# Kernel tuning notes

Measured on AMD Instinct MI355X. Metric: run time of the kernel, lower is better.

Reference implementation:

```python
import jax, jax.numpy as jnp
import numpy as np

D_MODEL = 1024
D_FF = 4 * D_MODEL
NUM_EXPERTS = 8
TOP_K = 2
BATCH, SEQ = 2, 2048


def setup_inputs() -> dict:
    key = jax.random.key(0)
    ks = jax.random.split(key, 6)
    s_in = 1.0 / np.sqrt(D_MODEL)
    s_ff = 1.0 / np.sqrt(D_FF)
    x = jax.random.normal(ks[0], (BATCH, SEQ, D_MODEL), dtype=jnp.float32)
    Wg = jax.random.uniform(ks[1], (D_MODEL, NUM_EXPERTS), minval=-s_in, maxval=s_in, dtype=jnp.float32)
    W1 = jax.random.uniform(ks[2], (NUM_EXPERTS, D_MODEL, D_FF), minval=-s_in, maxval=s_in, dtype=jnp.float32)
    b1 = jax.random.uniform(ks[3], (NUM_EXPERTS, D_FF), minval=-s_in, maxval=s_in, dtype=jnp.float32)
    W2 = jax.random.uniform(ks[4], (NUM_EXPERTS, D_FF, D_MODEL), minval=-s_ff, maxval=s_ff, dtype=jnp.float32)
    b2 = jax.random.uniform(ks[5], (NUM_EXPERTS, D_MODEL), minval=-s_ff, maxval=s_ff, dtype=jnp.float32)
    return {"x": x, "Wg": Wg, "W1": W1, "b1": b1, "W2": W2, "b2": b2}


def reference(x, Wg, W1, b1, W2, b2):
    B, S, D = x.shape
    x_flat = x.reshape(-1, D)                      # [T, D]
    gate_logits = x_flat @ Wg                      # [T, E] (eval mode: no noise)
    gate_probs = jax.nn.softmax(gate_logits, axis=-1)
    top_v, top_i = jax.lax.top_k(gate_probs, TOP_K)            # [T, k]
    top_v = top_v / (jnp.sum(top_v, axis=-1, keepdims=True) + 1e-8)
    out = jnp.zeros_like(x_flat)
    for e in range(NUM_EXPERTS):
        # combine weight for expert e: sum of normalized top-k probs routed here
        w_e = jnp.sum(jnp.where(top_i == e, top_v, 0.0), axis=-1)   # [T]
        h = jax.nn.gelu(x_flat @ W1[e] + b1[e], approximate=False)  # [T, F]
        y = h @ W2[e] + b2[e]                                       # [T, D]
        out = out + w_e[:, None] * y
    return out.reshape(B, S, D)
```

## Files before the change

kernel.cpp:

```cpp
#include <hip/hip_runtime.h>
#include <math.h>

typedef __attribute__((ext_vector_type(8))) short short8;
typedef __attribute__((ext_vector_type(4))) float f32x4;
typedef unsigned short u16;

#define NT 4096
#define DM 1024
#define DF 4096
#define NE 8
#define HROWS 9216
#define TIT 72
#define YROWS (2 * NT + 8)

static __device__ __forceinline__ u16 f2bf(float f) {
  union { float f; unsigned u; } v; v.f = f;
  return (u16)((v.u + 0x7fffu + ((v.u >> 16) & 1u)) >> 16);
}

static __device__ __forceinline__ void gload16(const void* g, void* l) {
  __builtin_amdgcn_global_load_lds((const __attribute__((address_space(1))) void*)g,
                                   (__attribute__((address_space(3))) void*)l, 16, 0, 0);
}

__global__ __launch_bounds__(256) void gate_k(const float* __restrict__ x,
                                              const float* __restrict__ Wg,
                                              int* __restrict__ te,
                                              float* __restrict__ tw) {
  int t = blockIdx.x * 4 + (threadIdx.x >> 6);
  int l = threadIdx.x & 63;
  float a0=0,a1=0,a2=0,a3=0,a4=0,a5=0,a6=0,a7=0;
  const float* xr = x + (size_t)t * DM;
  for (int k = l; k < DM; k += 64) {
    float xv = xr[k];
    const float4* wp = (const float4*)(Wg + k * 8);
    float4 w0 = wp[0], w1 = wp[1];
    a0 += xv * w0.x; a1 += xv * w0.y; a2 += xv * w0.z; a3 += xv * w0.w;
    a4 += xv * w1.x; a5 += xv * w1.y; a6 += xv * w1.z; a7 += xv * w1.w;
  }
#pragma unroll
  for (int s = 32; s >= 1; s >>= 1) {
    a0 += __shfl_down(a0, s); a1 += __shfl_down(a1, s);
    a2 += __shfl_down(a2, s); a3 += __shfl_down(a3, s);
    a4 += __shfl_down(a4, s); a5 += __shfl_down(a5, s);
    a6 += __shfl_down(a6, s); a7 += __shfl_down(a7, s);
  }
  if (l == 0) {
    float lg[8] = {a0,a1,a2,a3,a4,a5,a6,a7};
    float m = lg[0];
#pragma unroll
    for (int e = 1; e < 8; ++e) m = fmaxf(m, lg[e]);
    float p[8], s = 0.f;
#pragma unroll
    for (int e = 0; e < 8; ++e) { p[e] = expf(lg[e] - m); s += p[e]; }
#pragma unroll
    for (int e = 0; e < 8; ++e) p[e] /= s;
    int i0 = 0; float v0 = p[0];
#pragma unroll
    for (int e = 1; e < 8; ++e) if (p[e] > v0) { v0 = p[e]; i0 = e; }
    int i1 = -1; float v1 = -1.f;
#pragma unroll
    for (int e = 0; e < 8; ++e) {
      if (e == i0) continue;
      if (p[e] > v1) { v1 = p[e]; i1 = e; }
    }
    float norm = v0 + v1 + 1e-8f;
    te[t*2]   = i0; te[t*2+1] = i1;
    tw[t*2]   = v0 / norm; tw[t*2+1] = v1 / norm;
  }
}

__global__ __launch_bounds__(256) void route_k(const int* __restrict__ te,
                                               const float* __restrict__ tw,
                                               int* __restrict__ meta,
                                               int* __restrict__ lt,
                                               float* __restrict__ lw) {
  int i = blockIdx.x * 256 + threadIdx.x;
  if (i >= NT * 2) return;
  int e = te[i];
  float w = tw[i];
  int pos = atomicAdd(&meta[e], 1);
  lt[e * NT + pos] = i;
  lw[e * NT + pos] = w;
}

__global__ __launch_bounds__(256) void finalize_k(int* __restrict__ meta,
                                                  int* __restrict__ lt,
                                                  float* __restrict__ lw) {
  __shared__ int s_cnt[8], s_pc[8];
  if (threadIdx.x == 0) {
    int base = 0, nt_ = 0;
    for (int e = 0; e < 8; ++e) {
      int c = meta[e];
      int pc = (c + 127) & ~127;
      s_cnt[e] = c; s_pc[e] = pc;
      meta[8 + e] = pc;
      meta[16 + e] = base;
      base += pc;
      for (int mt = 0; mt < pc / 128; ++mt) meta[32 + nt_++] = (e << 16) | mt;
    }
    meta[24] = nt_;
  }
  __syncthreads();
  for (int e = 0; e < 8; ++e) {
    int c = s_cnt[e], pc = s_pc[e];
    for (int i = c + (int)threadIdx.x; i < pc; i += 256) {
      lt[e * NT + i] = 2 * NT;
      lw[e * NT + i] = 0.f;
    }
  }
}

__global__ __launch_bounds__(256) void prep_x(const float* __restrict__ x, u16* __restrict__ xbf) {
  size_t i = (size_t)blockIdx.x * 256 + threadIdx.x;
  const float4* p = (const float4*)(x + i * 8);
  float4 a = p[0], b = p[1];
  short8 o = { (short)f2bf(a.x), (short)f2bf(a.y), (short)f2bf(a.z), (short)f2bf(a.w),
               (short)f2bf(b.x), (short)f2bf(b.y), (short)f2bf(b.z), (short)f2bf(b.w) };
  *(short8*)(xbf + i * 8) = o;
}

__global__ __launch_bounds__(256) void prep_wT(const float* __restrict__ in,
                                               u16* __restrict__ out, int K, int N) {
  const int e = blockIdx.z;
  const int n0 = blockIdx.x * 64, k0 = blockIdx.y * 64;
  const float* ie = in + (size_t)e * K * N;
  u16* oe = out + (size_t)e * K * N;
  __shared__ u16 t[64 * 72];
  const int tid = threadIdx.x;
  const int kr = tid >> 4, nq = (tid & 15) * 4;
#pragma unroll
  for (int it = 0; it < 4; ++it) {
    int k = it * 16 + kr;
    float4 v = *(const float4*)(ie + (size_t)(k0 + k) * N + n0 + nq);
    t[(nq + 0) * 72 + k] = f2bf(v.x);
    t[(nq + 1) * 72 + k] = f2bf(v.y);
    t[(nq + 2) * 72 + k] = f2bf(v.z);
    t[(nq + 3) * 72 + k] = f2bf(v.w);
  }
  __syncthreads();
#pragma unroll
  for (int it = 0; it < 2; ++it) {
    int idx = it * 256 + tid;
    int n = idx >> 3, kc = idx & 7;
    short8 v = *(const short8*)&t[n * 72 + kc * 8];
    *(short8*)(oe + (size_t)(n0 + n) * K + k0 + kc * 8) = v;
  }
}

#define STAGE4(b)                                            \
  do {                                                       \
    gload16(pa0, laA + (b) * 4096 + lda0);                   \
    gload16(pa1, laA + (b) * 4096 + lda1);                   \
    gload16(pb0, laB + (b) * 4096 + lda0);                   \
    gload16(pb1, laB + (b) * 4096 + lda1);                   \
    pa0 += 32; pa1 += 32; pb0 += 32; pb1 += 32;              \
  } while (0)

__global__ __launch_bounds__(256) void ffn1_k(const u16* __restrict__ xbf,
                                              const u16* __restrict__ W1T,
                                              const float* __restrict__ b1,
                                              const int* __restrict__ lt,
                                              const int* __restrict__ meta,
                                              u16* __restrict__ H) {
  const int nt = blockIdx.x;
  const int ti = blockIdx.y;
  if (ti >= meta[24]) return;
  const int em = meta[32 + ti];
  const int e = em >> 16, mt = em & 0xffff;
  const int rbase = meta[16 + e];

  __shared__ u16 As[2 * 4096];
  __shared__ u16 Bs[2 * 4096];

  const int tid = threadIdx.x, lane = tid & 63, wv = tid >> 6;
  const int wm = wv >> 1, wn = wv & 1, l15 = lane & 15, l4 = lane >> 4;

  int r0i = tid >> 2, s0 = tid & 3;
  int r1i = (256 + tid) >> 2, s1 = s0;
  int kg0 = s0 ^ ((r0i >> 1) & 3);
  int kg1 = s1 ^ ((r1i >> 1) & 3);
  int tok0 = lt[e * NT + mt * 128 + r0i] >> 1; if (tok0 >= NT) tok0 = 0;
  int tok1 = lt[e * NT + mt * 128 + r1i] >> 1; if (tok1 >= NT) tok1 = 0;
  const u16* pa0 = xbf + (size_t)tok0 * DM + kg0 * 8;
  const u16* pa1 = xbf + (size_t)tok1 * DM + kg1 * 8;
  const u16* pb0 = W1T + ((size_t)e * DF + nt * 128 + r0i) * DM + kg0 * 8;
  const u16* pb1 = W1T + ((size_t)e * DF + nt * 128 + r1i) * DM + kg1 * 8;
  u16* laA = As; u16* laB = Bs;
  const int lda0 = (wv * 64) * 8, lda1 = (256 + wv * 64) * 8;

  int aoff[4], boff[4];
#pragma unroll
  for (int i = 0; i < 4; ++i) {
    int ra = wm * 64 + i * 16 + l15;
    aoff[i] = ra * 32 + (l4 ^ ((ra >> 1) & 3)) * 8;
    int rb = wn * 64 + i * 16 + l15;
    boff[i] = rb * 32 + (l4 ^ ((rb >> 1) & 3)) * 8;
  }

  f32x4 acc[4][4];
#pragma unroll
  for (int mi = 0; mi < 4; ++mi)
#pragma unroll
    for (int ni = 0; ni < 4; ++ni) acc[mi][ni] = 0.f;

  STAGE4(0);
  asm volatile("s_waitcnt vmcnt(0)" ::: "memory");
  __builtin_amdgcn_s_barrier();

  const int NK = DM / 32;
  int cur = 0;
  for (int ks = 0; ks < NK; ++ks) {
    if (ks + 1 < NK) STAGE4(cur ^ 1);
    short8 af[4], bf_[4];
#pragma unroll
    for (int i = 0; i < 4; ++i) {
      af[i]  = *(const short8*)&As[cur * 4096 + aoff[i]];
      bf_[i] = *(const short8*)&Bs[cur * 4096 + boff[i]];
    }
#pragma unroll
    for (int mi = 0; mi < 4; ++mi)
#pragma unroll
      for (int ni = 0; ni < 4; ++ni)
        acc[mi][ni] = __builtin_amdgcn_mfma_f32_16x16x32_bf16(af[mi], bf_[ni], acc[mi][ni], 0, 0, 0);
    asm volatile("s_waitcnt vmcnt(0)" ::: "memory");
    __builtin_amdgcn_s_barrier();
    cur ^= 1;
  }

  const size_t hrow0 = (size_t)rbase + mt * 128;
#pragma unroll
  for (int mi = 0; mi < 4; ++mi) {
#pragma unroll
    for (int ni = 0; ni < 4; ++ni) {
      int gn = nt * 128 + wn * 64 + ni * 16 + l15;
      float bias = b1[e * DF + gn];
      int rr = wm * 64 + mi * 16 + l4 * 4;
#pragma unroll
      for (int j = 0; j < 4; ++j) {
        float v = acc[mi][ni][j] + bias;
        v = 0.5f * v * (1.0f + erff(v * 0.70710678118654752f));
        H[(hrow0 + rr + j) * DF + gn] = f2bf(v);
      }
    }
  }
}

template <bool USEY>
__global__ __launch_bounds__(256) void ffn2_k(const u16* __restrict__ H,
                                              const u16* __restrict__ W2T,
                                              const float* __restrict__ b2,
                                              const int* __restrict__ lt,
                                              const float* __restrict__ lw,
                                              const int* __restrict__ meta,
                                              float* __restrict__ Y,
                                              float* __restrict__ out) {
  const int nt = blockIdx.x;
  const int ti = blockIdx.y;
  if (ti >= meta[24]) return;
  const int kz = blockIdx.z, nz = gridDim.z;
  const int em = meta[32 + ti];
  const int e = em >> 16, mt = em & 0xffff;
  const int rbase = meta[16 + e];
  const int KLEN = DF / nz, KOFF = kz * KLEN;

  __shared__ u16 As[2 * 4096];
  __shared__ u16 Bs[2 * 4096];
  __shared__ int s_ts[128];
  __shared__ float s_w[128];

  const int tid = threadIdx.x, lane = tid & 63, wv = tid >> 6;
  const int wm = wv >> 1, wn = wv & 1, l15 = lane & 15, l4 = lane >> 4;

  if (tid < 128) {
    s_ts[tid] = lt[e * NT + mt * 128 + tid];
    s_w[tid]  = lw[e * NT + mt * 128 + tid];
  }

  int r0i = tid >> 2, s0 = tid & 3;
  int r1i = (256 + tid) >> 2;
  int kg0 = s0 ^ ((r0i >> 1) & 3);
  int kg1 = s0 ^ ((r1i >> 1) & 3);
  const u16* pa0 = H + ((size_t)rbase + mt * 128 + r0i) * DF + KOFF + kg0 * 8;
  const u16* pa1 = H + ((size_t)rbase + mt * 128 + r1i) * DF + KOFF + kg1 * 8;
  const u16* pb0 = W2T + ((size_t)e * DM + nt * 128 + r0i) * DF + KOFF + kg0 * 8;
  const u16* pb1 = W2T + ((size_t)e * DM + nt * 128 + r1i) * DF + KOFF + kg1 * 8;
  u16* laA = As; u16* laB = Bs;
  const int lda0 = (wv * 64) * 8, lda1 = (256 + wv * 64) * 8;

  int aoff[4], boff[4];
#pragma unroll
  for (int i = 0; i < 4; ++i) {
    int ra = wm * 64 + i * 16 + l15;
    aoff[i] = ra * 32 + (l4 ^ ((ra >> 1) & 3)) * 8;
    int rb = wn * 64 + i * 16 + l15;
    boff[i] = rb * 32 + (l4 ^ ((rb >> 1) & 3)) * 8;
  }

  f32x4 acc[4][4];
#pragma unroll
  for (int mi = 0; mi < 4; ++mi)
#pragma unroll
    for (int ni = 0; ni < 4; ++ni) acc[mi][ni] = 0.f;

  STAGE4(0);
  asm volatile("s_waitcnt vmcnt(0)" ::: "memory");
  __builtin_amdgcn_s_barrier();

  const int NK = KLEN / 32;
  int cur = 0;
  for (int ks = 0; ks < NK; ++ks) {
    if (ks + 1 < NK) STAGE4(cur ^ 1);
    short8 af[4], bf_[4];
#pragma unroll
    for (int i = 0; i < 4; ++i) {
      af[i]  = *(const short8*)&As[cur * 4096 + aoff[i]];
      bf_[i] = *(const short8*)&Bs[cur * 4096 + boff[i]];
    }
#pragma unroll
    for (int mi = 0; mi < 4; ++mi)
#pragma unroll
      for (int ni = 0; ni < 4; ++ni)
        acc[mi][ni] = __builtin_amdgcn_mfma_f32_16x16x32_bf16(af[mi], bf_[ni], acc[mi][ni], 0, 0, 0);
    asm volatile("s_waitcnt vmcnt(0)" ::: "memory");
    __builtin_amdgcn_s_barrier();
    cur ^= 1;
  }

#pragma unroll
  for (int mi = 0; mi < 4; ++mi) {
#pragma unroll
    for (int ni = 0; ni < 4; ++ni) {
      int gn = nt * 128 + wn * 64 + ni * 16 + l15;
      float bias = (kz == 0) ? b2[e * DM + gn] : 0.f;
      int rr = wm * 64 + mi * 16 + l4 * 4;
#pragma unroll
      for (int j = 0; j < 4; ++j) {
        int r = rr + j;
        float w = s_w[r];
        int ts = s_ts[r];
        float v = w * (acc[mi][ni][j] + bias);
        if (USEY) {
          Y[((size_t)kz * YROWS + ts) * DM + gn] = v;
        } else {
          int tok = ts >> 1;
          if (tok >= NT) tok = 0;
          atomicAdd(out + (size_t)tok * DM + gn, v);
        }
      }
    }
  }
}

__global__ __launch_bounds__(256) void combine_k(const float* __restrict__ Y,
                                                 float* __restrict__ out, int nz) {
  size_t i4 = (size_t)blockIdx.x * 256 + threadIdx.x;
  size_t t = i4 >> 8;
  int c4 = (int)(i4 & 255) * 4;
  const float4 a = *(const float4*)(Y + (2 * t) * DM + c4);
  const float4 b = *(const float4*)(Y + (2 * t + 1) * DM + c4);
  float4 o = { a.x + b.x, a.y + b.y, a.z + b.z, a.w + b.w };
  if (nz == 2) {
    const float4 c = *(const float4*)(Y + ((size_t)YROWS + 2 * t) * DM + c4);
    const float4 d = *(const float4*)(Y + ((size_t)YROWS + 2 * t + 1) * DM + c4);
    o.x += c.x + d.x; o.y += c.y + d.y; o.z += c.z + d.z; o.w += c.w + d.w;
  }
  *(float4*)(out + t * DM + c4) = o;
}

extern "C" void kernel_launch(void* const* d_in, const int* in_sizes, int n_in,
                              void* d_out, int out_size, void* d_ws, size_t ws_size,
                              hipStream_t stream) {
  const float* x  = (const float*)d_in[0];
  const float* Wg = (const float*)d_in[1];
  const float* W1 = (const float*)d_in[2];
  const float* b1 = (const float*)d_in[3];
  const float* W2 = (const float*)d_in[4];
  const float* b2 = (const float*)d_in[5];
  float* out = (float*)d_out;

  char* ws = (char*)d_ws;
  size_t o = 0;
  auto take = [&](size_t sz) { size_t p = o; o = (o + sz + 1023) & ~(size_t)1023; return p; };

  int*   meta = (int*)(ws + take(1024));
  int*   te   = (int*)(ws + take((size_t)NT * 2 * 4));
  float* tw   = (float*)(ws + take((size_t)NT * 2 * 4));
  int*   lt   = (int*)(ws + take((size_t)NE * NT * 4));
  float* lw   = (float*)(ws + take((size_t)NE * NT * 4));
  u16*   xbf  = (u16*)(ws + take((size_t)NT * DM * 2));
  u16*   W1T  = (u16*)(ws + take((size_t)NE * DM * DF * 2));
  u16*   H    = (u16*)(ws + take((size_t)HROWS * DF * 2));
  size_t needB = o;
  size_t ySz = (size_t)YROWS * DM * 4;
  size_t needA  = needB + ((size_t)NE * DM * DF * 2 + 1024) + (ySz + 1024);
  size_t needA2 = needA + ySz + 1024;

  int nz = (ws_size >= needA2) ? 2 : (ws_size >= needA ? 1 : 0);
  u16*   W2T;
  float* Y = nullptr;
  if (nz > 0) {
    W2T = (u16*)(ws + take((size_t)NE * DM * DF * 2));
    Y   = (float*)(ws + take((size_t)nz * ySz));
  } else {
    W2T = W1T;
  }

  hipMemsetAsync(meta, 0, 1024, stream);
  if (nz == 0) hipMemsetAsync(out, 0, (size_t)NT * DM * 4, stream);

  gate_k<<<NT / 4, 256, 0, stream>>>(x, Wg, te, tw);
  route_k<<<(NT * 2) / 256, 256, 0, stream>>>(te, tw, meta, lt, lw);
  finalize_k<<<1, 256, 0, stream>>>(meta, lt, lw);
  prep_x<<<(NT * DM / 8) / 256, 256, 0, stream>>>(x, xbf);
  prep_wT<<<dim3(DF / 64, DM / 64, NE), 256, 0, stream>>>(W1, W1T, DM, DF);
  if (nz > 0)
    prep_wT<<<dim3(DM / 64, DF / 64, NE), 256, 0, stream>>>(W2, W2T, DF, DM);

  ffn1_k<<<dim3(DF / 128, TIT), 256, 0, stream>>>(xbf, W1T, b1, lt, meta, H);

  if (nz == 0)
    prep_wT<<<dim3(DM / 64, DF / 64, NE), 256, 0, stream>>>(W2, W2T, DF, DM);

  if (nz > 0) {
    ffn2_k<true><<<dim3(DM / 128, TIT, nz), 256, 0, stream>>>(H, W2T, b2, lt, lw, meta, Y, out);
    combine_k<<<NT, 256, 0, stream>>>(Y, out, nz);
  } else {
    ffn2_k<false><<<dim3(DM / 128, TIT, 1), 256, 0, stream>>>(H, W2T, b2, lt, lw, meta, Y, out);
  }
}
```

Baseline: 420.2 us.

## Fuse x bf16 cast into gate, swizzle blocks across XCDs, fast GELU, drop split-K

The bf16 conversion of x moves into the gating kernel, so the separate prep_x launch and its extra read of x go away. Both FFN kernels now take a 1D grid that is remapped so consecutive tiles land on the same XCD, for better L2 reuse. The exact erf GELU becomes a sigmoid-style approximation built from v_exp/v_rcp, which changes numerics slightly. Split-K for ffn2 is removed, giving fewer, longer blocks and a cheaper combine step, at the cost of less parallelism when there are few tiles.

```diff
diff --git a/kernel.cpp b/kernel.cpp
--- a/kernel.cpp
+++ b/kernel.cpp
@@ -18,15 +18,31 @@
   return (u16)((v.u + 0x7fffu + ((v.u >> 16) & 1u)) >> 16);
 }
 
+static __device__ __forceinline__ float fast_gelu(float x) {
+  float x2 = x * x;
+  float z = x * __builtin_fmaf(x2, 0.1029392294f, 2.302118131f);
+  float e, r;
+  asm("v_exp_f32 %0, %1" : "=v"(e) : "v"(z));
+  float e1 = e + 1.0f;
+  asm("v_rcp_f32 %0, %1" : "=v"(r) : "v"(e1));
+  return __builtin_fmaf(-x, r, x);
+}
+
 static __device__ __forceinline__ void gload16(const void* g, void* l) {
   __builtin_amdgcn_global_load_lds((const __attribute__((address_space(1))) void*)g,
                                    (__attribute__((address_space(3))) void*)l, 16, 0, 0);
 }
 
+static __device__ __forceinline__ int xcd_swz(int bid, int nwg) {
+  int per = nwg >> 3;
+  return (bid & 7) * per + (bid >> 3);
+}
+
 __global__ __launch_bounds__(256) void gate_k(const float* __restrict__ x,
                                               const float* __restrict__ Wg,
                                               int* __restrict__ te,
-                                              float* __restrict__ tw) {
+                                              float* __restrict__ tw,
+                                              u16* __restrict__ xbf) {
   int t = blockIdx.x * 4 + (threadIdx.x >> 6);
   int l = threadIdx.x & 63;
   float a0=0,a1=0,a2=0,a3=0,a4=0,a5=0,a6=0,a7=0;
@@ -37,6 +53,16 @@
     float4 w0 = wp[0], w1 = wp[1];
     a0 += xv * w0.x; a1 += xv * w0.y; a2 += xv * w0.z; a3 += xv * w0.w;
     a4 += xv * w1.x; a5 += xv * w1.y; a6 += xv * w1.z; a7 += xv * w1.w;
+  }
+  u16* xo = xbf + (size_t)t * DM;
+#pragma unroll
+  for (int h = 0; h < 2; ++h) {
+    int k = h * 512 + l * 8;
+    float4 a = *(const float4*)(xr + k);
+    float4 b = *(const float4*)(xr + k + 4);
+    short8 o8 = { (short)f2bf(a.x), (short)f2bf(a.y), (short)f2bf(a.z), (short)f2bf(a.w),
+                  (short)f2bf(b.x), (short)f2bf(b.y), (short)f2bf(b.z), (short)f2bf(b.w) };
+    *(short8*)(xo + k) = o8;
   }
 #pragma unroll
   for (int s = 32; s >= 1; s >>= 1) {
@@ -111,15 +137,6 @@
   }
 }
 
-__global__ __launch_bounds__(256) void prep_x(const float* __restrict__ x, u16* __restrict__ xbf) {
-  size_t i = (size_t)blockIdx.x * 256 + threadIdx.x;
-  const float4* p = (const float4*)(x + i * 8);
-  float4 a = p[0], b = p[1];
-  short8 o = { (short)f2bf(a.x), (short)f2bf(a.y), (short)f2bf(a.z), (short)f2bf(a.w),
-               (short)f2bf(b.x), (short)f2bf(b.y), (short)f2bf(b.z), (short)f2bf(b.w) };
-  *(short8*)(xbf + i * 8) = o;
-}
-
 __global__ __launch_bounds__(256) void prep_wT(const float* __restrict__ in,
                                                u16* __restrict__ out, int K, int N) {
   const int e = blockIdx.z;
@@ -163,8 +180,9 @@
                                               const int* __restrict__ lt,
                                               const int* __restrict__ meta,
                                               u16* __restrict__ H) {
-  const int nt = blockIdx.x;
-  const int ti = blockIdx.y;
+  const int vid = xcd_swz(blockIdx.x, (DF / 128) * TIT);
+  const int nt = vid & 31;
+  const int ti = vid >> 5;
   if (ti >= meta[24]) return;
   const int em = meta[32 + ti];
   const int e = em >> 16, mt = em & 0xffff;
@@ -177,9 +195,9 @@
   const int wm = wv >> 1, wn = wv & 1, l15 = lane & 15, l4 = lane >> 4;
 
   int r0i = tid >> 2, s0 = tid & 3;
-  int r1i = (256 + tid) >> 2, s1 = s0;
+  int r1i = (256 + tid) >> 2;
   int kg0 = s0 ^ ((r0i >> 1) & 3);
-  int kg1 = s1 ^ ((r1i >> 1) & 3);
+  int kg1 = s0 ^ ((r1i >> 1) & 3);
   int tok0 = lt[e * NT + mt * 128 + r0i] >> 1; if (tok0 >= NT) tok0 = 0;
   int tok1 = lt[e * NT + mt * 128 + r1i] >> 1; if (tok1 >= NT) tok1 = 0;
   const u16* pa0 = xbf + (size_t)tok0 * DM + kg0 * 8;
@@ -238,8 +256,7 @@
       int rr = wm * 64 + mi * 16 + l4 * 4;
 #pragma unroll
       for (int j = 0; j < 4; ++j) {
-        float v = acc[mi][ni][j] + bias;
-        v = 0.5f * v * (1.0f + erff(v * 0.70710678118654752f));
+        float v = fast_gelu(acc[mi][ni][j] + bias);
         H[(hrow0 + rr + j) * DF + gn] = f2bf(v);
       }
     }
@@ -255,14 +272,13 @@
                                               const int* __restrict__ meta,
                                               float* __restrict__ Y,
                                               float* __restrict__ out) {
-  const int nt = blockIdx.x;
-  const int ti = blockIdx.y;
+  const int vid = xcd_swz(blockIdx.x, (DM / 128) * TIT);
+  const int nt = vid & 7;
+  const int ti = vid >> 3;
   if (ti >= meta[24]) return;
-  const int kz = blockIdx.z, nz = gridDim.z;
   const int em = meta[32 + ti];
   const int e = em >> 16, mt = em & 0xffff;
   const int rbase = meta[16 + e];
-  const int KLEN = DF / nz, KOFF = kz * KLEN;
 
   __shared__ u16 As[2 * 4096];
   __shared__ u16 Bs[2 * 4096];
@@ -281,10 +297,10 @@
   int r1i = (256 + tid) >> 2;
   int kg0 = s0 ^ ((r0i >> 1) & 3);
   int kg1 = s0 ^ ((r1i >> 1) & 3);
-  const u16* pa0 = H + ((size_t)rbase + mt * 128 + r0i) * DF + KOFF + kg0 * 8;
-  const u16* pa1 = H + ((size_t)rbase + mt * 128 + r1i) * DF + KOFF + kg1 * 8;
-  const u16* pb0 = W2T + ((size_t)e * DM + nt * 128 + r0i) * DF + KOFF + kg0 * 8;
-  const u16* pb1 = W2T + ((size_t)e * DM + nt * 128 + r1i) * DF + KOFF + kg1 * 8;
+  const u16* pa0 = H + ((size_t)rbase + mt * 128 + r0i) * DF + kg0 * 8;
+  const u16* pa1 = H + ((size_t)rbase + mt * 128 + r1i) * DF + kg1 * 8;
+  const u16* pb0 = W2T + ((size_t)e * DM + nt * 128 + r0i) * DF + kg0 * 8;
+  const u16* pb1 = W2T + ((size_t)e * DM + nt * 128 + r1i) * DF + kg1 * 8;
   u16* laA = As; u16* laB = Bs;
   const int lda0 = (wv * 64) * 8, lda1 = (256 + wv * 64) * 8;
 
@@ -307,7 +323,7 @@
   asm volatile("s_waitcnt vmcnt(0)" ::: "memory");
   __builtin_amdgcn_s_barrier();
 
-  const int NK = KLEN / 32;
+  const int NK = DF / 32;
   int cur = 0;
   for (int ks = 0; ks < NK; ++ks) {
     if (ks + 1 < NK) STAGE4(cur ^ 1);
@@ -332,7 +348,7 @@
 #pragma unroll
     for (int ni = 0; ni < 4; ++ni) {
       int gn = nt * 128 + wn * 64 + ni * 16 + l15;
-      float bias = (kz == 0) ? b2[e * DM + gn] : 0.f;
+      float bias = b2[e * DM + gn];
       int rr = wm * 64 + mi * 16 + l4 * 4;
 #pragma unroll
       for (int j = 0; j < 4; ++j) {
@@ -341,7 +357,7 @@
         int ts = s_ts[r];
         float v = w * (acc[mi][ni][j] + bias);
         if (USEY) {
-          Y[((size_t)kz * YROWS + ts) * DM + gn] = v;
+          Y[(size_t)ts * DM + gn] = v;
         } else {
           int tok = ts >> 1;
           if (tok >= NT) tok = 0;
@@ -353,18 +369,13 @@
 }
 
 __global__ __launch_bounds__(256) void combine_k(const float* __restrict__ Y,
-                                                 float* __restrict__ out, int nz) {
+                                                 float* __restrict__ out) {
   size_t i4 = (size_t)blockIdx.x * 256 + threadIdx.x;
   size_t t = i4 >> 8;
   int c4 = (int)(i4 & 255) * 4;
   const float4 a = *(const float4*)(Y + (2 * t) * DM + c4);
   const float4 b = *(const float4*)(Y + (2 * t + 1) * DM + c4);
   float4 o = { a.x + b.x, a.y + b.y, a.z + b.z, a.w + b.w };
-  if (nz == 2) {
-    const float4 c = *(const float4*)(Y + ((size_t)YROWS + 2 * t) * DM + c4);
-    const float4 d = *(const float4*)(Y + ((size_t)YROWS + 2 * t + 1) * DM + c4);
-    o.x += c.x + d.x; o.y += c.y + d.y; o.z += c.z + d.z; o.w += c.w + d.w;
-  }
   *(float4*)(out + t * DM + c4) = o;
 }
 
@@ -393,39 +404,37 @@
   u16*   H    = (u16*)(ws + take((size_t)HROWS * DF * 2));
   size_t needB = o;
   size_t ySz = (size_t)YROWS * DM * 4;
-  size_t needA  = needB + ((size_t)NE * DM * DF * 2 + 1024) + (ySz + 1024);
-  size_t needA2 = needA + ySz + 1024;
-
-  int nz = (ws_size >= needA2) ? 2 : (ws_size >= needA ? 1 : 0);
+  size_t needA = needB + ((size_t)NE * DM * DF * 2 + 1024) + (ySz + 1024);
+
+  bool pathA = (ws_size >= needA);
   u16*   W2T;
   float* Y = nullptr;
-  if (nz > 0) {
+  if (pathA) {
     W2T = (u16*)(ws + take((size_t)NE * DM * DF * 2));
-    Y   = (float*)(ws + take((size_t)nz * ySz));
+    Y   = (float*)(ws + take(ySz));
   } else {
     W2T = W1T;
   }
 
   hipMemsetAsync(meta, 0, 1024, stream);
-  if (nz == 0) hipMemsetAsync(out, 0, (size_t)NT * DM * 4, stream);
-
-  gate_k<<<NT / 4, 256, 0, stream>>>(x, Wg, te, tw);
+  if (!pathA) hipMemsetAsync(out, 0, (size_t)NT * DM * 4, stream);
+
+  gate_k<<<NT / 4, 256, 0, stream>>>(x, Wg, te, tw, xbf);
   route_k<<<(NT * 2) / 256, 256, 0, stream>>>(te, tw, meta, lt, lw);
   finalize_k<<<1, 256, 0, stream>>>(meta, lt, lw);
-  prep_x<<<(NT * DM / 8) / 256, 256, 0, stream>>>(x, xbf);
   prep_wT<<<dim3(DF / 64, DM / 64, NE), 256, 0, stream>>>(W1, W1T, DM, DF);
-  if (nz > 0)
+  if (pathA)
     prep_wT<<<dim3(DM / 64, DF / 64, NE), 256, 0, stream>>>(W2, W2T, DF, DM);
 
-  ffn1_k<<<dim3(DF / 128, TIT), 256, 0, stream>>>(xbf, W1T, b1, lt, meta, H);
-
-  if (nz == 0)
+  ffn1_k<<<(DF / 128) * TIT, 256, 0, stream>>>(xbf, W1T, b1, lt, meta, H);
+
+  if (!pathA)
     prep_wT<<<dim3(DM / 64, DF / 64, NE), 256, 0, stream>>>(W2, W2T, DF, DM);
 
-  if (nz > 0) {
-    ffn2_k<true><<<dim3(DM / 128, TIT, nz), 256, 0, stream>>>(H, W2T, b2, lt, lw, meta, Y, out);
-    combine_k<<<NT, 256, 0, stream>>>(Y, out, nz);
+  if (pathA) {
+    ffn2_k<true><<<(DM / 128) * TIT, 256, 0, stream>>>(H, W2T, b2, lt, lw, meta, Y, out);
+    combine_k<<<NT, 256, 0, stream>>>(Y, out);
   } else {
-    ffn2_k<false><<<dim3(DM / 128, TIT, 1), 256, 0, stream>>>(H, W2T, b2, lt, lw, meta, Y, out);
-  }
-}
+    ffn2_k<false><<<(DM / 128) * TIT, 256, 0, stream>>>(H, W2T, b2, lt, lw, meta, Y, out);
+  }
+}
```

New measurement: 406.1 us. 3.4% less time.
